# Optimization experiments

Hardware: AMD Instinct MI355X
Metric: run time of the kernel (lower is better)

## Reference

```python
import jax, jax.numpy as jnp
import numpy as np

# dims matching init_kwargs
NC_IN, NC_OUT = 32, 32
M_IN, M_OUT = 3, 3          # to_order(degree)=2*d+1 with degree=1
NUM_FREQ = 3                # to_order(min(degree_in, degree_out))
EDGE_DIM, MID_DIM = 32, 64  # mid_dim = int(edge_dim * radial_mult)
RAD_OUT = NUM_FREQ * NC_IN * NC_OUT  # 3072
LN_EPS = 1e-5


def _layernorm(x, g, b):
    mu = jnp.mean(x, axis=-1, keepdims=True)
    var = jnp.var(x, axis=-1, keepdims=True)
    return (x - mu) * jax.lax.rsqrt(var + LN_EPS) * g + b


def setup_inputs() -> dict:
    key = jax.random.key(0)
    ks = jax.random.split(key, 8)
    B, N, K = 1, 1024, 32
    edges = jax.random.normal(ks[0], (B, N, K, EDGE_DIM), dtype=jnp.float32)
    feats = jax.random.normal(ks[1], (B, N, K, NC_IN, M_IN), dtype=jnp.float32)
    basis = jax.random.normal(ks[2], (B * N * K, M_IN, NUM_FREQ * M_OUT), dtype=jnp.float32)
    # radial MLP params (Linear -> LN -> GELU) x2, then Linear (no bias since dropout=0)
    s1 = 1.0 / np.sqrt(EDGE_DIM)
    s2 = 1.0 / np.sqrt(MID_DIM)
    W1 = jax.random.uniform(ks[3], (EDGE_DIM, MID_DIM), jnp.float32, -s1, s1)
    b1 = jnp.zeros((MID_DIM,), jnp.float32)
    g1 = jnp.ones((MID_DIM,), jnp.float32)
    beta1 = jnp.zeros((MID_DIM,), jnp.float32)
    W2 = jax.random.uniform(ks[4], (MID_DIM, MID_DIM), jnp.float32, -s2, s2)
    b2 = jnp.zeros((MID_DIM,), jnp.float32)
    g2 = jnp.ones((MID_DIM,), jnp.float32)
    beta2 = jnp.zeros((MID_DIM,), jnp.float32)
    W3 = jax.random.uniform(ks[5], (MID_DIM, RAD_OUT), jnp.float32, -s2, s2)
    return dict(edges=edges, feats=feats, basis=basis, W1=W1, b1=b1, g1=g1,
                beta1=beta1, W2=W2, b2=b2, g2=g2, beta2=beta2, W3=W3)


def reference(edges, feats, basis, W1, b1, g1, beta1, W2, b2, g2, beta2, W3):
    B, N, K = feats.shape[:3]
    E = B * N * K
    # radial MLP: (E, edge_dim) -> (E, nc_out * nc_in * num_freq)
    x = edges.reshape(E, EDGE_DIM)
    h = jax.nn.gelu(_layernorm(x @ W1 + b1, g1, beta1), approximate=False)
    h = jax.nn.gelu(_layernorm(h @ W2 + b2, g2, beta2), approximate=False)
    rw = (h @ W3).reshape(E, NC_OUT, NC_IN * NUM_FREQ)  # rearrange '(o i f)' then flatten
    # feats @ basis: (E, nc_in, m_in) @ (E, m_in, num_freq*m_out)
    f = feats.reshape(E, NC_IN, M_IN)
    tmp = jnp.matmul(f, basis).reshape(E, NC_IN * NUM_FREQ, M_OUT)
    out = jnp.matmul(rw, tmp)  # (E, nc_out, m_out)
    return out.reshape(B, N, K, NC_OUT, M_OUT)
```

## Files before the change

kernel.cpp:

```cpp
#include <hip/hip_runtime.h>
#include <cstdint>
#include <cstddef>

typedef __bf16 bf8 __attribute__((ext_vector_type(8)));
typedef float f32x4 __attribute__((ext_vector_type(4)));
typedef float f32x2 __attribute__((ext_vector_type(2)));
typedef float f32x4u __attribute__((ext_vector_type(4), aligned(4)));
typedef float f32x3u __attribute__((ext_vector_type(3), aligned(4)));
typedef unsigned short us8 __attribute__((ext_vector_type(8)));
typedef unsigned short us4 __attribute__((ext_vector_type(4)));
typedef unsigned int u32x4 __attribute__((ext_vector_type(4)));
typedef unsigned int u32x2 __attribute__((ext_vector_type(2)));

__device__ __forceinline__ uint16_t f2b(float f) {
    uint32_t u = __builtin_bit_cast(uint32_t, f);
    u += 0x7FFFu + ((u >> 16) & 1u);
    return (uint16_t)(u >> 16);
}
__device__ __forceinline__ float b2f(uint16_t h) {
    uint32_t u = ((uint32_t)h) << 16;
    return __builtin_bit_cast(float, u);
}
#if __has_builtin(__builtin_amdgcn_cvt_pk_bf16_f32)
__device__ __forceinline__ uint32_t pkbf(float a, float b) {
    auto r = __builtin_amdgcn_cvt_pk_bf16_f32(a, b);
    return __builtin_bit_cast(uint32_t, r);
}
#else
__device__ __forceinline__ uint32_t pkbf(float a, float b) {
    return (uint32_t)f2b(a) | ((uint32_t)f2b(b) << 16);
}
#endif
__device__ __forceinline__ f32x2 up01(uint32_t d) {
    f32x2 r;
    r[0] = __builtin_bit_cast(float, d << 16);
    r[1] = __builtin_bit_cast(float, d & 0xffff0000u);
    return r;
}
__device__ __forceinline__ float gelu_fast(float y) {
    float y3 = y * y * y;
    float z2 = 1.5957691216f * (y + 0.044715f * y3);
    float u = __expf(-z2);
    return y * __builtin_amdgcn_rcpf(1.0f + u);
}

#define MFMA(a, b, c) __builtin_amdgcn_mfma_f32_16x16x32_bf16( \
    __builtin_bit_cast(bf8, (a)), __builtin_bit_cast(bf8, (b)), (c), 0, 0, 0)

__global__ void prep_weights(const float* __restrict__ W1,
                             const float* __restrict__ W2,
                             const float* __restrict__ W3,
                             uint16_t* __restrict__ wt) {
    __shared__ float tile[32][33];
    int bx = blockIdx.x;
    if (bx < 192) {
        int kb = (bx & 1) * 32;
        int jb = (bx >> 1) * 32;
        int tx = threadIdx.x & 31, ty = threadIdx.x >> 5;
        #pragma unroll
        for (int l = 0; l < 4; ++l)
            tile[ty + 8 * l][tx] = W3[(size_t)(kb + ty + 8 * l) * 3072 + jb + tx];
        __syncthreads();
        #pragma unroll
        for (int l = 0; l < 4; ++l) {
            int j = jb + ty + 8 * l;
            wt[6144 + (size_t)j * 64 + kb + tx] = f2b(tile[tx][ty + 8 * l]);
        }
    } else {
        int t = (bx - 192) * 256 + threadIdx.x;
        if (t < 2048) {
            int i = t >> 6, j = t & 63;
            wt[j * 32 + i] = f2b(W1[t]);
        } else {
            int t2 = t - 2048;
            int k = t2 >> 6, j = t2 & 63;
            wt[2048 + j * 64 + k] = f2b(W2[t2]);
        }
    }
}

__global__ __launch_bounds__(256, 3) void pairconv_main(
    const float* __restrict__ edges, const float* __restrict__ feats,
    const float* __restrict__ basis,
    const float* __restrict__ b1, const float* __restrict__ g1, const float* __restrict__ be1,
    const float* __restrict__ b2, const float* __restrict__ g2, const float* __restrict__ be2,
    const uint16_t* __restrict__ wt, float* __restrict__ out) {

    __shared__ __align__(16) uint32_t sh_t01[64 * 100];
    __shared__ __align__(16) uint16_t sh_t2[64 * 104];
    __shared__ __align__(16) uint16_t sh_h[4][16 * 64];

    const int tid = threadIdx.x;
    const int e0 = blockIdx.x * 64;
    const int lane = tid & 63, w = tid >> 6;
    const int n = lane & 15, q = lane >> 4;

    const int eb = e0 + w * 16;
    f32x4 ex0 = *(const f32x4*)(edges + (size_t)(eb + n) * 32 + q * 8);
    f32x4 ex1 = *(const f32x4*)(edges + (size_t)(eb + n) * 32 + q * 8 + 4);

    #pragma unroll
    for (int it = 0; it < 8; ++it) {
        int idx = tid + it * 256;
        int e = idx >> 5, i = idx & 31;
        f32x3u fv = *(const f32x3u*)(feats + ((size_t)(e0 + e) * 32 + i) * 3);
        const float* bpp = basis + (size_t)(e0 + e) * 27;
        float bp[27];
        #pragma unroll
        for (int v = 0; v < 6; ++v) {
            f32x4u t = *(const f32x4u*)(bpp + v * 4);
            bp[v * 4] = t[0]; bp[v * 4 + 1] = t[1]; bp[v * 4 + 2] = t[2]; bp[v * 4 + 3] = t[3];
        }
        bp[24] = bpp[24]; bp[25] = bpp[25]; bp[26] = bpp[26];
        #pragma unroll
        for (int f = 0; f < 3; ++f) {
            int c = i * 3 + f;
            float v0 = fv[0] * bp[f * 3 + 0] + fv[1] * bp[9 + f * 3 + 0] + fv[2] * bp[18 + f * 3 + 0];
            float v1 = fv[0] * bp[f * 3 + 1] + fv[1] * bp[9 + f * 3 + 1] + fv[2] * bp[18 + f * 3 + 1];
            float v2 = fv[0] * bp[f * 3 + 2] + fv[1] * bp[9 + f * 3 + 2] + fv[2] * bp[18 + f * 3 + 2];
            sh_t01[e * 100 + c] = pkbf(v0, v1);
            sh_t2[e * 104 + c]  = (uint16_t)pkbf(v2, v2);
        }
    }

    {
        us8 bx;
        {
            u32x4 bxp;
            bxp[0] = pkbf(ex0[0], ex0[1]); bxp[1] = pkbf(ex0[2], ex0[3]);
            bxp[2] = pkbf(ex1[0], ex1[1]); bxp[3] = pkbf(ex1[2], ex1[3]);
            bx = __builtin_bit_cast(us8, bxp);
        }
        f32x4 acc[4];
        #pragma unroll
        for (int mt = 0; mt < 4; ++mt) {
            us8 a = *(const us8*)(wt + (mt * 16 + n) * 32 + q * 8);
            f32x4 z = {0.f, 0.f, 0.f, 0.f};
            acc[mt] = MFMA(a, bx, z);
        }
        float v[4][4];
        float s1 = 0.f, s2 = 0.f;
        #pragma unroll
        for (int mt = 0; mt < 4; ++mt) {
            f32x4 bb = *(const f32x4*)&b1[mt * 16 + q * 4];
            #pragma unroll
            for (int r = 0; r < 4; ++r) {
                float x = acc[mt][r] + bb[r];
                v[mt][r] = x; s1 += x; s2 += x * x;
            }
        }
        s1 += __shfl_xor(s1, 16, 64); s1 += __shfl_xor(s1, 32, 64);
        s2 += __shfl_xor(s2, 16, 64); s2 += __shfl_xor(s2, 32, 64);
        float mean = s1 * (1.f / 64.f);
        float var  = s2 * (1.f / 64.f) - mean * mean;
        float rs = __builtin_amdgcn_rsqf(var + 1e-5f);
        #pragma unroll
        for (int mt = 0; mt < 4; ++mt) {
            f32x4 gg = *(const f32x4*)&g1[mt * 16 + q * 4];
            f32x4 be = *(const f32x4*)&be1[mt * 16 + q * 4];
            float y0 = gelu_fast((v[mt][0] - mean) * rs * gg[0] + be[0]);
            float y1 = gelu_fast((v[mt][1] - mean) * rs * gg[1] + be[1]);
            float y2 = gelu_fast((v[mt][2] - mean) * rs * gg[2] + be[2]);
            float y3 = gelu_fast((v[mt][3] - mean) * rs * gg[3] + be[3]);
            u32x2 pk; pk[0] = pkbf(y0, y1); pk[1] = pkbf(y2, y3);
            int kq = mt * 2 + (q >> 1);
            *(u32x2*)&sh_h[w][n * 64 + ((kq ^ (n & 7)) << 3) + (q & 1) * 4] = pk;
        }
    }
    {
        us8 bh0 = *(const us8*)&sh_h[w][n * 64 + ((q ^ (n & 7)) << 3)];
        us8 bh1 = *(const us8*)&sh_h[w][n * 64 + (((4 + q) ^ (n & 7)) << 3)];
        f32x4 acc[4];
        #pragma unroll
        for (int mt = 0; mt < 4; ++mt) {
            us8 a0 = *(const us8*)(wt + 2048 + (mt * 16 + n) * 64 + q * 8);
            us8 a1 = *(const us8*)(wt + 2048 + (mt * 16 + n) * 64 + 32 + q * 8);
            f32x4 z = {0.f, 0.f, 0.f, 0.f};
            acc[mt] = MFMA(a0, bh0, z);
            acc[mt] = MFMA(a1, bh1, acc[mt]);
        }
        float v[4][4]; float s1 = 0.f, s2 = 0.f;
        #pragma unroll
        for (int mt = 0; mt < 4; ++mt) {
            f32x4 bb = *(const f32x4*)&b2[mt * 16 + q * 4];
            #pragma unroll
            for (int r = 0; r < 4; ++r) {
                float x = acc[mt][r] + bb[r];
                v[mt][r] = x; s1 += x; s2 += x * x;
            }
        }
        s1 += __shfl_xor(s1, 16, 64); s1 += __shfl_xor(s1, 32, 64);
        s2 += __shfl_xor(s2, 16, 64); s2 += __shfl_xor(s2, 32, 64);
        float mean = s1 * (1.f / 64.f);
        float var  = s2 * (1.f / 64.f) - mean * mean;
        float rs = __builtin_amdgcn_rsqf(var + 1e-5f);
        #pragma unroll
        for (int mt = 0; mt < 4; ++mt) {
            f32x4 gg = *(const f32x4*)&g2[mt * 16 + q * 4];
            f32x4 be = *(const f32x4*)&be2[mt * 16 + q * 4];
            float y0 = gelu_fast((v[mt][0] - mean) * rs * gg[0] + be[0]);
            float y1 = gelu_fast((v[mt][1] - mean) * rs * gg[1] + be[1]);
            float y2 = gelu_fast((v[mt][2] - mean) * rs * gg[2] + be[2]);
            float y3 = gelu_fast((v[mt][3] - mean) * rs * gg[3] + be[3]);
            u32x2 pk; pk[0] = pkbf(y0, y1); pk[1] = pkbf(y2, y3);
            int kq = mt * 2 + (q >> 1);
            *(u32x2*)&sh_h[w][n * 64 + ((kq ^ (n & 7)) << 3) + (q & 1) * 4] = pk;
        }
    }
    __syncthreads();

    {
        const uint16_t* w3t = wt + 6144;
        us8 bh[4][2];
        #pragma unroll
        for (int nt = 0; nt < 4; ++nt) {
            bh[nt][0] = *(const us8*)&sh_h[nt][n * 64 + ((q ^ (n & 7)) << 3)];
            bh[nt][1] = *(const us8*)&sh_h[nt][n * 64 + (((4 + q) ^ (n & 7)) << 3)];
        }
        const int ob = w * 8;
        #pragma unroll 1
        for (int oc = 0; oc < 2; ++oc) {
            f32x2 p01[4][4];
            float p2v[4][4];
            #pragma unroll
            for (int op = 0; op < 4; ++op)
                #pragma unroll
                for (int nt = 0; nt < 4; ++nt) {
                    p01[op][nt] = (f32x2){0.f, 0.f}; p2v[op][nt] = 0.f;
                }

            #pragma unroll 1
            for (int mt = 0; mt < 6; ++mt) {
                us8 a[4][2];
                const uint16_t* apb = w3t +
                    (size_t)((ob + oc * 4) * 96 + mt * 16 + n) * 64 + q * 8;
                #pragma unroll
                for (int op = 0; op < 4; ++op) {
                    a[op][0] = *(const us8*)(apb + (size_t)op * 6144);
                    a[op][1] = *(const us8*)(apb + (size_t)op * 6144 + 32);
                }
                #pragma unroll
                for (int nt = 0; nt < 4; ++nt) {
                    int e = nt * 16 + n;
                    u32x4 d  = *(const u32x4*)&sh_t01[e * 100 + mt * 16 + q * 4];
                    us4 t2   = *(const us4*)&sh_t2[e * 104 + mt * 16 + q * 4];
                    f32x2 f01[4]; float fm2[4];
                    #pragma unroll
                    for (int r = 0; r < 4; ++r) {
                        f01[r] = up01(d[r]);
                        fm2[r] = b2f(t2[r]);
                    }
                    #pragma unroll
                    for (int op = 0; op < 4; ++op) {
                        f32x4 z = {0.f, 0.f, 0.f, 0.f};
                        f32x4 acc = MFMA(a[op][0], bh[nt][0], z);
                        acc = MFMA(a[op][1], bh[nt][1], acc);
                        #pragma unroll
                        for (int r = 0; r < 4; ++r) {
                            p01[op][nt] += f01[r] * acc[r];
                            p2v[op][nt] += fm2[r] * acc[r];
                        }
                    }
                }
            }
            #pragma unroll
            for (int nt = 0; nt < 4; ++nt) {
                #pragma unroll
                for (int op = 0; op < 4; ++op) {
                    int o = ob + oc * 4 + op;
                    float v0 = p01[op][nt][0], v1 = p01[op][nt][1], v2 = p2v[op][nt];
                    v0 += __shfl_xor(v0, 16, 64); v0 += __shfl_xor(v0, 32, 64);
                    v1 += __shfl_xor(v1, 16, 64); v1 += __shfl_xor(v1, 32, 64);
                    v2 += __shfl_xor(v2, 16, 64); v2 += __shfl_xor(v2, 32, 64);
                    float val = (q == 0) ? v0 : ((q == 1) ? v1 : v2);
                    if (q < 3)
                        out[(size_t)(e0 + nt * 16 + n) * 96 + o * 3 + q] = val;
                }
            }
        }
    }
}

extern "C" void kernel_launch(void* const* d_in, const int* in_sizes, int n_in,
                              void* d_out, int out_size, void* d_ws, size_t ws_size,
                              hipStream_t stream) {
    const float* edges = (const float*)d_in[0];
    const float* feats = (const float*)d_in[1];
    const float* basis = (const float*)d_in[2];
    const float* W1  = (const float*)d_in[3];
    const float* b1  = (const float*)d_in[4];
    const float* g1  = (const float*)d_in[5];
    const float* be1 = (const float*)d_in[6];
    const float* W2  = (const float*)d_in[7];
    const float* b2  = (const float*)d_in[8];
    const float* g2  = (const float*)d_in[9];
    const float* be2 = (const float*)d_in[10];
    const float* W3  = (const float*)d_in[11];
    uint16_t* wt = (uint16_t*)d_ws;
    float* out = (float*)d_out;

    const int E = in_sizes[0] / 32;
    hipLaunchKernelGGL(prep_weights, dim3(216), dim3(256), 0, stream, W1, W2, W3, wt);
    hipLaunchKernelGGL(pairconv_main, dim3(E / 64), dim3(256), 0, stream,
                       edges, feats, basis, b1, g1, be1, b2, g2, be2, wt, out);
}
```

Before: 129.9 us.

## Split MLP into separate kernel and halve output channels per conv block

Moves the two-layer radial MLP into its own kernel that writes the bf16 hidden activations to workspace. The convolution kernel then runs two blocks per 64-edge tile, each handling half of the output channels. This doubles the grid and raises the occupancy hint to 4 blocks per CU. Feats loads are now vectorised per edge quarter, and outputs are staged through shared memory so global stores are coalesced. The cost is an extra launch, a round trip of the hidden activations through global memory, and the feats-times-basis product being recomputed in both half-blocks.

```diff
diff --git a/kernel.cpp b/kernel.cpp
--- a/kernel.cpp
+++ b/kernel.cpp
@@ -6,7 +6,6 @@
 typedef float f32x4 __attribute__((ext_vector_type(4)));
 typedef float f32x2 __attribute__((ext_vector_type(2)));
 typedef float f32x4u __attribute__((ext_vector_type(4), aligned(4)));
-typedef float f32x3u __attribute__((ext_vector_type(3), aligned(4)));
 typedef unsigned short us8 __attribute__((ext_vector_type(8)));
 typedef unsigned short us4 __attribute__((ext_vector_type(4)));
 typedef unsigned int u32x4 __attribute__((ext_vector_type(4)));
@@ -46,6 +45,8 @@
 
 #define MFMA(a, b, c) __builtin_amdgcn_mfma_f32_16x16x32_bf16( \
     __builtin_bit_cast(bf8, (a)), __builtin_bit_cast(bf8, (b)), (c), 0, 0, 0)
+
+#define H_OFF 202752
 
 __global__ void prep_weights(const float* __restrict__ W1,
                              const float* __restrict__ W2,
@@ -79,58 +80,29 @@
     }
 }
 
-__global__ __launch_bounds__(256, 3) void pairconv_main(
-    const float* __restrict__ edges, const float* __restrict__ feats,
-    const float* __restrict__ basis,
+__global__ __launch_bounds__(64) void mlp_kernel(
+    const float* __restrict__ edges,
     const float* __restrict__ b1, const float* __restrict__ g1, const float* __restrict__ be1,
     const float* __restrict__ b2, const float* __restrict__ g2, const float* __restrict__ be2,
-    const uint16_t* __restrict__ wt, float* __restrict__ out) {
-
-    __shared__ __align__(16) uint32_t sh_t01[64 * 100];
-    __shared__ __align__(16) uint16_t sh_t2[64 * 104];
-    __shared__ __align__(16) uint16_t sh_h[4][16 * 64];
-
-    const int tid = threadIdx.x;
-    const int e0 = blockIdx.x * 64;
-    const int lane = tid & 63, w = tid >> 6;
+    const uint16_t* __restrict__ wt, uint16_t* __restrict__ h_g) {
+
+    __shared__ __align__(16) uint16_t sh_h1[16 * 64];
+
+    const int lane = threadIdx.x;
     const int n = lane & 15, q = lane >> 4;
-
-    const int eb = e0 + w * 16;
+    const int eb = blockIdx.x * 16;
+
     f32x4 ex0 = *(const f32x4*)(edges + (size_t)(eb + n) * 32 + q * 8);
     f32x4 ex1 = *(const f32x4*)(edges + (size_t)(eb + n) * 32 + q * 8 + 4);
 
-    #pragma unroll
-    for (int it = 0; it < 8; ++it) {
-        int idx = tid + it * 256;
-        int e = idx >> 5, i = idx & 31;
-        f32x3u fv = *(const f32x3u*)(feats + ((size_t)(e0 + e) * 32 + i) * 3);
-        const float* bpp = basis + (size_t)(e0 + e) * 27;
-        float bp[27];
-        #pragma unroll
-        for (int v = 0; v < 6; ++v) {
-            f32x4u t = *(const f32x4u*)(bpp + v * 4);
-            bp[v * 4] = t[0]; bp[v * 4 + 1] = t[1]; bp[v * 4 + 2] = t[2]; bp[v * 4 + 3] = t[3];
-        }
-        bp[24] = bpp[24]; bp[25] = bpp[25]; bp[26] = bpp[26];
-        #pragma unroll
-        for (int f = 0; f < 3; ++f) {
-            int c = i * 3 + f;
-            float v0 = fv[0] * bp[f * 3 + 0] + fv[1] * bp[9 + f * 3 + 0] + fv[2] * bp[18 + f * 3 + 0];
-            float v1 = fv[0] * bp[f * 3 + 1] + fv[1] * bp[9 + f * 3 + 1] + fv[2] * bp[18 + f * 3 + 1];
-            float v2 = fv[0] * bp[f * 3 + 2] + fv[1] * bp[9 + f * 3 + 2] + fv[2] * bp[18 + f * 3 + 2];
-            sh_t01[e * 100 + c] = pkbf(v0, v1);
-            sh_t2[e * 104 + c]  = (uint16_t)pkbf(v2, v2);
-        }
-    }
-
-    {
-        us8 bx;
-        {
-            u32x4 bxp;
-            bxp[0] = pkbf(ex0[0], ex0[1]); bxp[1] = pkbf(ex0[2], ex0[3]);
-            bxp[2] = pkbf(ex1[0], ex1[1]); bxp[3] = pkbf(ex1[2], ex1[3]);
-            bx = __builtin_bit_cast(us8, bxp);
-        }
+    us8 bx;
+    {
+        u32x4 bxp;
+        bxp[0] = pkbf(ex0[0], ex0[1]); bxp[1] = pkbf(ex0[2], ex0[3]);
+        bxp[2] = pkbf(ex1[0], ex1[1]); bxp[3] = pkbf(ex1[2], ex1[3]);
+        bx = __builtin_bit_cast(us8, bxp);
+    }
+    {
         f32x4 acc[4];
         #pragma unroll
         for (int mt = 0; mt < 4; ++mt) {
@@ -138,8 +110,7 @@
             f32x4 z = {0.f, 0.f, 0.f, 0.f};
             acc[mt] = MFMA(a, bx, z);
         }
-        float v[4][4];
-        float s1 = 0.f, s2 = 0.f;
+        float v[4][4]; float s1 = 0.f, s2 = 0.f;
         #pragma unroll
         for (int mt = 0; mt < 4; ++mt) {
             f32x4 bb = *(const f32x4*)&b1[mt * 16 + q * 4];
@@ -164,12 +135,12 @@
             float y3 = gelu_fast((v[mt][3] - mean) * rs * gg[3] + be[3]);
             u32x2 pk; pk[0] = pkbf(y0, y1); pk[1] = pkbf(y2, y3);
             int kq = mt * 2 + (q >> 1);
-            *(u32x2*)&sh_h[w][n * 64 + ((kq ^ (n & 7)) << 3) + (q & 1) * 4] = pk;
-        }
-    }
-    {
-        us8 bh0 = *(const us8*)&sh_h[w][n * 64 + ((q ^ (n & 7)) << 3)];
-        us8 bh1 = *(const us8*)&sh_h[w][n * 64 + (((4 + q) ^ (n & 7)) << 3)];
+            *(u32x2*)&sh_h1[n * 64 + ((kq ^ (n & 7)) << 3) + (q & 1) * 4] = pk;
+        }
+    }
+    {
+        us8 bh0 = *(const us8*)&sh_h1[n * 64 + ((q ^ (n & 7)) << 3)];
+        us8 bh1 = *(const us8*)&sh_h1[n * 64 + (((4 + q) ^ (n & 7)) << 3)];
         f32x4 acc[4];
         #pragma unroll
         for (int mt = 0; mt < 4; ++mt) {
@@ -203,80 +174,142 @@
             float y2 = gelu_fast((v[mt][2] - mean) * rs * gg[2] + be[2]);
             float y3 = gelu_fast((v[mt][3] - mean) * rs * gg[3] + be[3]);
             u32x2 pk; pk[0] = pkbf(y0, y1); pk[1] = pkbf(y2, y3);
-            int kq = mt * 2 + (q >> 1);
-            *(u32x2*)&sh_h[w][n * 64 + ((kq ^ (n & 7)) << 3) + (q & 1) * 4] = pk;
-        }
+            *(u32x2*)(h_g + (size_t)(eb + n) * 64 + mt * 16 + q * 4) = pk;
+        }
+    }
+}
+
+__global__ __launch_bounds__(256, 4) void conv_kernel(
+    const float* __restrict__ feats, const float* __restrict__ basis,
+    const uint16_t* __restrict__ wt, const uint16_t* __restrict__ h_g,
+    float* __restrict__ out) {
+
+    __shared__ __align__(16) uint32_t sh_t01[64 * 100];
+    __shared__ __align__(16) uint16_t sh_t2[64 * 104];
+
+    const int tid = threadIdx.x;
+    const int e0 = (blockIdx.x >> 1) * 64;
+    const int half = blockIdx.x & 1;
+
+    {
+        const int e = tid >> 2, iq = tid & 3;
+        f32x4 fv[6];
+        const float* fp = feats + (size_t)(e0 + e) * 96 + iq * 24;
+        #pragma unroll
+        for (int l = 0; l < 6; ++l) fv[l] = *(const f32x4*)(fp + l * 4);
+        float bp[27];
+        const float* bpp = basis + (size_t)(e0 + e) * 27;
+        #pragma unroll
+        for (int v = 0; v < 6; ++v) {
+            f32x4u t = *(const f32x4u*)(bpp + v * 4);
+            bp[v * 4] = t[0]; bp[v * 4 + 1] = t[1]; bp[v * 4 + 2] = t[2]; bp[v * 4 + 3] = t[3];
+        }
+        bp[24] = bpp[24]; bp[25] = bpp[25]; bp[26] = bpp[26];
+
+        uint32_t t01b[24]; uint16_t t2b[24];
+        const float* fvs = (const float*)fv;
+        #pragma unroll
+        for (int ii = 0; ii < 8; ++ii) {
+            float a0 = fvs[ii * 3], a1 = fvs[ii * 3 + 1], a2 = fvs[ii * 3 + 2];
+            #pragma unroll
+            for (int f = 0; f < 3; ++f) {
+                float v0 = a0 * bp[f * 3 + 0] + a1 * bp[9 + f * 3 + 0] + a2 * bp[18 + f * 3 + 0];
+                float v1 = a0 * bp[f * 3 + 1] + a1 * bp[9 + f * 3 + 1] + a2 * bp[18 + f * 3 + 1];
+                float v2 = a0 * bp[f * 3 + 2] + a1 * bp[9 + f * 3 + 2] + a2 * bp[18 + f * 3 + 2];
+                t01b[ii * 3 + f] = pkbf(v0, v1);
+                t2b[ii * 3 + f]  = (uint16_t)pkbf(v2, v2);
+            }
+        }
+        #pragma unroll
+        for (int l = 0; l < 6; ++l)
+            *(u32x4*)&sh_t01[e * 100 + iq * 24 + l * 4] = *(u32x4*)&t01b[l * 4];
+        #pragma unroll
+        for (int l = 0; l < 3; ++l)
+            *(us8*)&sh_t2[e * 104 + iq * 24 + l * 8] = *(us8*)&t2b[l * 8];
     }
     __syncthreads();
 
+    const int lane = tid & 63, w = tid >> 6;
+    const int n = lane & 15, q = lane >> 4;
     {
         const uint16_t* w3t = wt + 6144;
         us8 bh[4][2];
         #pragma unroll
         for (int nt = 0; nt < 4; ++nt) {
-            bh[nt][0] = *(const us8*)&sh_h[nt][n * 64 + ((q ^ (n & 7)) << 3)];
-            bh[nt][1] = *(const us8*)&sh_h[nt][n * 64 + (((4 + q) ^ (n & 7)) << 3)];
-        }
-        const int ob = w * 8;
+            const uint16_t* hp = h_g + (size_t)(e0 + nt * 16 + n) * 64 + q * 8;
+            bh[nt][0] = *(const us8*)hp;
+            bh[nt][1] = *(const us8*)(hp + 32);
+        }
+        const int ob = half * 16 + w * 4;
+        f32x2 p01[4][4];
+        float p2v[4][4];
+        #pragma unroll
+        for (int op = 0; op < 4; ++op)
+            #pragma unroll
+            for (int nt = 0; nt < 4; ++nt) {
+                p01[op][nt] = (f32x2){0.f, 0.f}; p2v[op][nt] = 0.f;
+            }
+
         #pragma unroll 1
-        for (int oc = 0; oc < 2; ++oc) {
-            f32x2 p01[4][4];
-            float p2v[4][4];
-            #pragma unroll
-            for (int op = 0; op < 4; ++op)
+        for (int mt = 0; mt < 6; ++mt) {
+            us8 a[4][2];
+            const uint16_t* apb = w3t + (size_t)(ob * 96 + mt * 16 + n) * 64 + q * 8;
+            #pragma unroll
+            for (int op = 0; op < 4; ++op) {
+                a[op][0] = *(const us8*)(apb + (size_t)op * 6144);
+                a[op][1] = *(const us8*)(apb + (size_t)op * 6144 + 32);
+            }
+            #pragma unroll
+            for (int nt = 0; nt < 4; ++nt) {
+                int e = nt * 16 + n;
+                u32x4 d  = *(const u32x4*)&sh_t01[e * 100 + mt * 16 + q * 4];
+                us4 t2   = *(const us4*)&sh_t2[e * 104 + mt * 16 + q * 4];
+                f32x2 f01[4]; float fm2[4];
                 #pragma unroll
-                for (int nt = 0; nt < 4; ++nt) {
-                    p01[op][nt] = (f32x2){0.f, 0.f}; p2v[op][nt] = 0.f;
+                for (int r = 0; r < 4; ++r) {
+                    f01[r] = up01(d[r]);
+                    fm2[r] = b2f(t2[r]);
                 }
-
-            #pragma unroll 1
-            for (int mt = 0; mt < 6; ++mt) {
-                us8 a[4][2];
-                const uint16_t* apb = w3t +
-                    (size_t)((ob + oc * 4) * 96 + mt * 16 + n) * 64 + q * 8;
                 #pragma unroll
                 for (int op = 0; op < 4; ++op) {
-                    a[op][0] = *(const us8*)(apb + (size_t)op * 6144);
-                    a[op][1] = *(const us8*)(apb + (size_t)op * 6144 + 32);
-                }
-                #pragma unroll
-                for (int nt = 0; nt < 4; ++nt) {
-                    int e = nt * 16 + n;
-                    u32x4 d  = *(const u32x4*)&sh_t01[e * 100 + mt * 16 + q * 4];
-                    us4 t2   = *(const us4*)&sh_t2[e * 104 + mt * 16 + q * 4];
-                    f32x2 f01[4]; float fm2[4];
+                    f32x4 z = {0.f, 0.f, 0.f, 0.f};
+                    f32x4 acc = MFMA(a[op][0], bh[nt][0], z);
+                    acc = MFMA(a[op][1], bh[nt][1], acc);
                     #pragma unroll
                     for (int r = 0; r < 4; ++r) {
-                        f01[r] = up01(d[r]);
-                        fm2[r] = b2f(t2[r]);
-                    }
-                    #pragma unroll
-                    for (int op = 0; op < 4; ++op) {
-                        f32x4 z = {0.f, 0.f, 0.f, 0.f};
-                        f32x4 acc = MFMA(a[op][0], bh[nt][0], z);
-                        acc = MFMA(a[op][1], bh[nt][1], acc);
-                        #pragma unroll
-                        for (int r = 0; r < 4; ++r) {
-                            p01[op][nt] += f01[r] * acc[r];
-                            p2v[op][nt] += fm2[r] * acc[r];
-                        }
+                        p01[op][nt] += f01[r] * acc[r];
+                        p2v[op][nt] += fm2[r] * acc[r];
                     }
                 }
             }
-            #pragma unroll
-            for (int nt = 0; nt < 4; ++nt) {
-                #pragma unroll
-                for (int op = 0; op < 4; ++op) {
-                    int o = ob + oc * 4 + op;
-                    float v0 = p01[op][nt][0], v1 = p01[op][nt][1], v2 = p2v[op][nt];
-                    v0 += __shfl_xor(v0, 16, 64); v0 += __shfl_xor(v0, 32, 64);
-                    v1 += __shfl_xor(v1, 16, 64); v1 += __shfl_xor(v1, 32, 64);
-                    v2 += __shfl_xor(v2, 16, 64); v2 += __shfl_xor(v2, 32, 64);
-                    float val = (q == 0) ? v0 : ((q == 1) ? v1 : v2);
-                    if (q < 3)
-                        out[(size_t)(e0 + nt * 16 + n) * 96 + o * 3 + q] = val;
-                }
-            }
+        }
+
+        __syncthreads();
+        float* shout = (float*)sh_t2;
+        #pragma unroll
+        for (int nt = 0; nt < 4; ++nt) {
+            #pragma unroll
+            for (int op = 0; op < 4; ++op) {
+                float v0 = p01[op][nt][0], v1 = p01[op][nt][1], v2 = p2v[op][nt];
+                v0 += __shfl_xor(v0, 16, 64); v0 += __shfl_xor(v0, 32, 64);
+                v1 += __shfl_xor(v1, 16, 64); v1 += __shfl_xor(v1, 32, 64);
+                v2 += __shfl_xor(v2, 16, 64); v2 += __shfl_xor(v2, 32, 64);
+                float val = (q == 0) ? v0 : ((q == 1) ? v1 : v2);
+                if (q < 3)
+                    shout[(nt * 16 + n) * 52 + (w * 4 + op) * 3 + q] = val;
+            }
+        }
+    }
+    __syncthreads();
+
+    {
+        const float* shout = (const float*)sh_t2;
+        int e = tid >> 2, j0 = (tid & 3) * 12;
+        float* op = out + (size_t)(e0 + e) * 96 + half * 48 + j0;
+        #pragma unroll
+        for (int l = 0; l < 3; ++l) {
+            f32x4 v = *(const f32x4*)&shout[e * 52 + j0 + l * 4];
+            *(f32x4*)(op + l * 4) = v;
         }
     }
 }
@@ -296,11 +329,14 @@
     const float* g2  = (const float*)d_in[9];
     const float* be2 = (const float*)d_in[10];
     const float* W3  = (const float*)d_in[11];
-    uint16_t* wt = (uint16_t*)d_ws;
+    uint16_t* wt  = (uint16_t*)d_ws;
+    uint16_t* h_g = wt + H_OFF;
     float* out = (float*)d_out;
 
     const int E = in_sizes[0] / 32;
     hipLaunchKernelGGL(prep_weights, dim3(216), dim3(256), 0, stream, W1, W2, W3, wt);
-    hipLaunchKernelGGL(pairconv_main, dim3(E / 64), dim3(256), 0, stream,
-                       edges, feats, basis, b1, g1, be1, b2, g2, be2, wt, out);
-}
+    hipLaunchKernelGGL(mlp_kernel, dim3(E / 16), dim3(64), 0, stream,
+                       edges, b1, g1, be1, b2, g2, be2, wt, h_g);
+    hipLaunchKernelGGL(conv_kernel, dim3((E / 64) * 2), dim3(256), 0, stream,
+                       feats, basis, wt, h_g, out);
+}
```

After: 167.0 us. 1.29x slower.
